# Kernel tuning notes

Hardware: AMD Instinct MI355X
Metric: run time of the kernel (lower is better)

Reference implementation:

```python
import jax, jax.numpy as jnp
import numpy as np

EPS = 1e-5

def conv1x1(x, W, b):
    # x: [B,Cin,H,W], W: [Cout,Cin], b: [Cout] -> [B,Cout,H,W]
    return jnp.einsum('oc,bchw->bohw', W, x) + b[None, :, None, None]

def setup_inputs() -> dict:
    key = jax.random.key(0)
    ks = jax.random.split(key, 12)
    C, Ci = 256, 128
    B, Hh, Wh, Hl, Wl = 8, 32, 32, 64, 64
    sc = 1.0 / np.sqrt(C)
    sci = 1.0 / np.sqrt(Ci)
    return {
        'x_high': jax.random.normal(ks[0], (B, C, Hh, Wh), jnp.float32),
        'x_low':  jax.random.normal(ks[1], (B, C, Hl, Wl), jnp.float32),
        'Wg': jax.random.normal(ks[2], (Ci, C), jnp.float32) * sc,
        'bg': jax.random.normal(ks[3], (Ci,), jnp.float32) * 0.01,
        'Wt': jax.random.normal(ks[4], (Ci, C), jnp.float32) * sc,
        'bt': jax.random.normal(ks[5], (Ci,), jnp.float32) * 0.01,
        'Wp': jax.random.normal(ks[6], (Ci, C), jnp.float32) * sc,
        'bp': jax.random.normal(ks[7], (Ci,), jnp.float32) * 0.01,
        'Wz': jax.random.normal(ks[8], (C, Ci), jnp.float32) * sci,
        'bz': jax.random.normal(ks[9], (C,), jnp.float32) * 0.01,
        'gamma': jnp.ones((C,), jnp.float32),
        'beta': jnp.zeros((C,), jnp.float32),
    }

def reference(x_high, x_low, Wg, bg, Wt, bt, Wp, bp, Wz, bz, gamma, beta):
    B, C, Hl, Wl = x_low.shape
    Ci = Wg.shape[0]
    Nh = x_high.shape[2] * x_high.shape[3]
    Nl = Hl * Wl
    # 1x1 conv projections (pure channel GEMMs)
    g_x = conv1x1(x_high, Wg, bg).reshape(B, Ci, Nh).transpose(0, 2, 1)    # [B,Nh,Ci]
    theta_x = conv1x1(x_low, Wt, bt).reshape(B, Ci, Nl).transpose(0, 2, 1) # [B,Nl,Ci]
    phi_x = conv1x1(x_high, Wp, bp).reshape(B, Ci, Nh)                     # [B,Ci,Nh]
    # unnormalized attention (no softmax), scaled by number of key positions
    f = jnp.matmul(theta_x, phi_x)            # [B,Nl,Nh]
    y = jnp.matmul(f / Nh, g_x)               # [B,Nl,Ci]
    y = y.transpose(0, 2, 1).reshape(B, Ci, Hl, Wl)
    # W_z: 1x1 conv then GroupNorm(num_groups=1) -> layernorm over (C,H,W) per sample
    z = conv1x1(y, Wz, bz)                    # [B,C,Hl,Wl]
    mu = jnp.mean(z, axis=(1, 2, 3), keepdims=True)
    var = jnp.var(z, axis=(1, 2, 3), keepdims=True)
    z = (z - mu) * jax.lax.rsqrt(var + EPS)
    z = z * gamma[None, :, None, None] + beta[None, :, None, None]
    return z
```

## Files before the change

kernel.cpp:

```cpp
#include <hip/hip_runtime.h>
#include <hip/hip_bf16.h>

typedef __attribute__((ext_vector_type(8))) short bf16x8;
typedef __attribute__((ext_vector_type(4))) float f32x4;
typedef __attribute__((ext_vector_type(8))) unsigned short us8;

#define MFMA(a, b, c) __builtin_amdgcn_mfma_f32_16x16x32_bf16(a, b, c, 0, 0, 0)

__device__ inline unsigned short f2bf(float f) {
  unsigned u = __builtin_bit_cast(unsigned, f);
  u += 0x7FFF + ((u >> 16) & 1);
  return (unsigned short)(u >> 16);
}
__device__ inline float bf2f(unsigned short s) {
  unsigned u = ((unsigned)s) << 16;
  return __builtin_bit_cast(float, u);
}
__device__ inline unsigned pack2(float lo, float hi) {
  return (unsigned)f2bf(lo) | ((unsigned)f2bf(hi) << 16);
}
__device__ inline void gll16(const unsigned short* gsrc, unsigned short* ldst) {
  __builtin_amdgcn_global_load_lds(
      (const __attribute__((address_space(1))) unsigned int*)gsrc,
      (__attribute__((address_space(3))) unsigned int*)ldst, 16, 0, 0);
}

__global__ __launch_bounds__(256) void proj_f2(
    const float* __restrict__ xh,
    const float* __restrict__ Wp, const float* __restrict__ bp,
    const float* __restrict__ Wg, const float* __restrict__ bg,
    unsigned short* __restrict__ phi,
    unsigned short* __restrict__ gg) {
  __shared__ unsigned short Bs[64 * 256];
  __shared__ unsigned short As[2][64 * 64];
  const int b = blockIdx.x, i0 = blockIdx.y * 64, n0 = blockIdx.z * 64;
  const int t = threadIdx.x, lane = t & 63;
  const int wid = t >> 6, wr = wid >> 1, wc = wid & 1;
  #pragma unroll
  for (int it = 0; it < 8; ++it) {
    int s = it * 256 + t;
    int nf = (s & 7) | ((s >> 10) << 3);
    int c2 = (s >> 3) & 127;
    const float* p = xh + ((size_t)(b * 256 + 2 * c2)) * 1024 + n0 + nf * 4;
    float4 a = *(const float4*)p;
    float4 bq = *(const float4*)(p + 1024);
    const float* ap = (const float*)&a;
    const float* bp2 = (const float*)&bq;
    #pragma unroll
    for (int i = 0; i < 4; ++i) {
      int n = nf * 4 + i;
      int col32 = (((c2 >> 2) ^ (n & 7)) << 2) | (c2 & 3);
      ((unsigned*)Bs)[n * 128 + col32] = pack2(ap[i], bp2[i]);
    }
  }
  f32x4 accP[2][2] = {};
  f32x4 accG[2][2] = {};
  const int ar = t >> 2, acb = (t & 3) * 16;
  for (int kt = 0; kt < 4; ++kt) {
    #pragma unroll
    for (int w = 0; w < 2; ++w) {
      const float* W = (w ? Wg : Wp) + (size_t)(i0 + ar) * 256 + kt * 64 + acb;
      #pragma unroll
      for (int q = 0; q < 4; ++q) {
        float4 v = *(const float4*)(W + q * 4);
        int cl0 = acb + q * 4;
        int c2a = cl0 >> 1, c2b = c2a + 1;
        int sa = (((c2a >> 2) ^ (ar & 7)) << 2) | (c2a & 3);
        int sb = (((c2b >> 2) ^ (ar & 7)) << 2) | (c2b & 3);
        ((unsigned*)As[w])[ar * 32 + sa] = pack2(v.x, v.y);
        ((unsigned*)As[w])[ar * 32 + sb] = pack2(v.z, v.w);
      }
    }
    __syncthreads();
    #pragma unroll
    for (int ks = 0; ks < 2; ++ks) {
      bf16x8 bfr[2];
      #pragma unroll
      for (int fm = 0; fm < 2; ++fm) {
        int r = wc * 32 + fm * 16 + (lane & 15);
        int gc = kt * 8 + ks * 4 + (lane >> 4);
        bfr[fm] = *(const bf16x8*)&Bs[r * 256 + (gc ^ (r & 7)) * 8];
      }
      #pragma unroll
      for (int fo = 0; fo < 2; ++fo) {
        int r = wr * 32 + fo * 16 + (lane & 15);
        int ga = ks * 4 + (lane >> 4);
        bf16x8 ap = *(const bf16x8*)&As[0][r * 64 + (ga ^ (r & 7)) * 8];
        bf16x8 ag = *(const bf16x8*)&As[1][r * 64 + (ga ^ (r & 7)) * 8];
        accP[fo][0] = MFMA(ap, bfr[0], accP[fo][0]);
        accP[fo][1] = MFMA(ap, bfr[1], accP[fo][1]);
        accG[fo][0] = MFMA(ag, bfr[0], accG[fo][0]);
        accG[fo][1] = MFMA(ag, bfr[1], accG[fo][1]);
      }
    }
    __syncthreads();
  }
  #pragma unroll
  for (int fo = 0; fo < 2; ++fo) {
    #pragma unroll
    for (int q = 0; q < 4; ++q) {
      int i = i0 + wr * 32 + fo * 16 + (lane >> 4) * 4 + q;
      float vp = bp[i], vg = bg[i];
      #pragma unroll
      for (int fm = 0; fm < 2; ++fm) {
        int n = n0 + wc * 32 + fm * 16 + (lane & 15);
        size_t off = ((size_t)((b * 128) + i)) * 1024 + n;
        phi[off] = f2bf(accP[fo][fm][q] + vp);
        gg[off]  = f2bf(accG[fo][fm][q] + vg);
      }
    }
  }
}

__global__ __launch_bounds__(256) void mpart_mfma(
    const unsigned short* __restrict__ phi, const unsigned short* __restrict__ gg,
    float* __restrict__ Mpart) {
  __shared__ unsigned short ps[128 * 128];
  __shared__ unsigned short gs[128 * 128];
  const int b = blockIdx.x, kc = blockIdx.y;
  const int t = threadIdx.x, lane = t & 63;
  const int wid = t >> 6, wr = wid >> 1, wc = wid & 1;
  #pragma unroll
  for (int j = 0; j < 8; ++j) {
    int slot = t + j * 256;
    int r = slot >> 4, gq = slot & 15;
    size_t src = ((size_t)(b * 128 + r)) * 1024 + kc * 128 + (gq ^ (r & 7)) * 8;
    gll16(phi + src, ps + slot * 8);
    gll16(gg + src, gs + slot * 8);
  }
  __syncthreads();
  f32x4 acc[4][4] = {};
  #pragma unroll
  for (int ks = 0; ks < 4; ++ks) {
    bf16x8 av[4], bv[4];
    #pragma unroll
    for (int f = 0; f < 4; ++f) {
      int ra = wr * 64 + f * 16 + (lane & 15);
      int rb = wc * 64 + f * 16 + (lane & 15);
      int gc = ks * 4 + (lane >> 4);
      av[f] = *(const bf16x8*)&ps[ra * 128 + (gc ^ (ra & 7)) * 8];
      bv[f] = *(const bf16x8*)&gs[rb * 128 + (gc ^ (rb & 7)) * 8];
    }
    #pragma unroll
    for (int i = 0; i < 4; ++i)
      #pragma unroll
      for (int j2 = 0; j2 < 4; ++j2)
        acc[i][j2] = MFMA(av[i], bv[j2], acc[i][j2]);
  }
  float* mp = Mpart + ((size_t)(b * 8 + kc)) * 128 * 128;
  #pragma unroll
  for (int i = 0; i < 4; ++i)
    #pragma unroll
    for (int q = 0; q < 4; ++q) {
      int ii = wr * 64 + i * 16 + (lane >> 4) * 4 + q;
      #pragma unroll
      for (int j2 = 0; j2 < 4; ++j2) {
        int jj = wc * 64 + j2 * 16 + (lane & 15);
        mp[ii * 128 + jj] = acc[i][j2][q];
      }
    }
}

__global__ __launch_bounds__(256) void mkw2(
    const float* __restrict__ Mpart, const float* __restrict__ Wz,
    const float* __restrict__ Wt, const float* __restrict__ bt,
    const float* __restrict__ bz,
    unsigned short* __restrict__ W2b, float* __restrict__ b2) {
  __shared__ float Ms[128 * 129];
  __shared__ float Ws2[32 * 132];
  const int b = blockIdx.x, o0 = blockIdx.y * 32;
  const int t = threadIdx.x;
  #pragma unroll
  for (int q = 0; q < 4; ++q) {
    int f = t + q * 256;
    int o = f >> 5, j4 = (f & 31) * 4;
    float4 v = *(const float4*)&Wz[(size_t)(o0 + o) * 128 + j4];
    Ws2[o * 132 + j4 + 0] = v.x; Ws2[o * 132 + j4 + 1] = v.y;
    Ws2[o * 132 + j4 + 2] = v.z; Ws2[o * 132 + j4 + 3] = v.w;
  }
  #pragma unroll
  for (int q = 0; q < 16; ++q) {
    int f = t + q * 256;
    const float4* p = (const float4*)(Mpart + (size_t)b * 8 * 16384) + f;
    float4 s = p[0];
    #pragma unroll
    for (int kc = 1; kc < 8; ++kc) {
      float4 v = p[(size_t)kc * 4096];
      s.x += v.x; s.y += v.y; s.z += v.z; s.w += v.w;
    }
    const float sc = 1.0f / 1024.0f;
    int i = f >> 5, j = (f & 31) * 4;
    Ms[i * 129 + j + 0] = s.x * sc; Ms[i * 129 + j + 1] = s.y * sc;
    Ms[i * 129 + j + 2] = s.z * sc; Ms[i * 129 + j + 3] = s.w * sc;
  }
  __syncthreads();
  const int i = t & 127, oh = t >> 7;
  float k2[16] = {};
  for (int j = 0; j < 128; ++j) {
    float m = Ms[i * 129 + j];
    #pragma unroll
    for (int oo = 0; oo < 16; ++oo)
      k2[oo] += m * Ws2[(oh * 16 + oo) * 132 + j];
  }
  __syncthreads();
  #pragma unroll
  for (int oo = 0; oo < 16; ++oo)
    Ws2[(oh * 16 + oo) * 132 + i] = k2[oo];
  __syncthreads();
  const int c = t;
  float acc[32] = {};
  for (int i2 = 0; i2 < 128; ++i2) {
    float wt = Wt[(size_t)i2 * 256 + c];
    #pragma unroll
    for (int o = 0; o < 32; ++o)
      acc[o] += wt * Ws2[o * 132 + i2];
  }
  #pragma unroll
  for (int o = 0; o < 32; ++o)
    W2b[((size_t)(b * 256 + o0 + o)) * 256 + c] = f2bf(acc[o]);
  if (t < 32) {
    float s = 0.f;
    for (int i2 = 0; i2 < 128; ++i2) s += Ws2[t * 132 + i2] * bt[i2];
    b2[b * 256 + o0 + t] = s + bz[o0 + t];
  }
}

__global__ __launch_bounds__(256) void mk_z_f(
    const float* __restrict__ xl,
    const unsigned short* __restrict__ W2b,
    const float* __restrict__ b2,
    unsigned short* __restrict__ z,
    float* __restrict__ sums) {
  __shared__ unsigned short As[256 * 64];
  __shared__ unsigned short Bs[32 * 64];
  __shared__ float red[8];
  const int b = blockIdx.x, m0 = blockIdx.y * 32;
  const int t = threadIdx.x, lane = t & 63;
  const int w = t >> 6;
  const int mf = t & 7, c2 = t >> 3;
  f32x4 acc[4][2] = {};
  for (int kt = 0; kt < 4; ++kt) {
    #pragma unroll
    for (int j = 0; j < 8; ++j) {
      int slot = t + j * 256;
      int r = slot >> 3, gq = slot & 7;
      gll16(W2b + ((size_t)(b * 256 + r)) * 256 + kt * 64 + (gq ^ (r & 7)) * 8,
            As + slot * 8);
    }
    {
      const float* p = xl + ((size_t)(b * 256 + kt * 64 + 2 * c2)) * 4096 + m0 + mf * 4;
      float4 a = *(const float4*)p;
      float4 bq = *(const float4*)(p + 4096);
      const float* ap = (const float*)&a;
      const float* bp2 = (const float*)&bq;
      #pragma unroll
      for (int i = 0; i < 4; ++i) {
        int m = mf * 4 + i;
        int col32 = (((c2 >> 2) ^ (m & 7)) << 2) | (c2 & 3);
        ((unsigned*)Bs)[m * 32 + col32] = pack2(ap[i], bp2[i]);
      }
    }
    __syncthreads();
    #pragma unroll
    for (int ks = 0; ks < 2; ++ks) {
      bf16x8 av[4], bv[2];
      #pragma unroll
      for (int f = 0; f < 2; ++f) {
        int rb = f * 16 + (lane & 15);
        int gc = ks * 4 + (lane >> 4);
        bv[f] = *(const bf16x8*)&Bs[rb * 64 + (gc ^ (rb & 7)) * 8];
      }
      #pragma unroll
      for (int f = 0; f < 4; ++f) {
        int ra = w * 64 + f * 16 + (lane & 15);
        int gc = ks * 4 + (lane >> 4);
        av[f] = *(const bf16x8*)&As[ra * 64 + (gc ^ (ra & 7)) * 8];
      }
      #pragma unroll
      for (int i = 0; i < 4; ++i)
        #pragma unroll
        for (int j2 = 0; j2 < 2; ++j2)
          acc[i][j2] = MFMA(av[i], bv[j2], acc[i][j2]);
    }
    __syncthreads();
  }
  float ls = 0.f, ls2 = 0.f;
  #pragma unroll
  for (int i = 0; i < 4; ++i) {
    #pragma unroll
    for (int q = 0; q < 4; ++q) {
      int o = w * 64 + i * 16 + (lane >> 4) * 4 + q;
      float bias = b2[b * 256 + o];
      #pragma unroll
      for (int j2 = 0; j2 < 2; ++j2) {
        int m = m0 + j2 * 16 + (lane & 15);
        float v = acc[i][j2][q] + bias;
        z[((size_t)(b * 256 + o)) * 4096 + m] = f2bf(v);
        ls += v; ls2 += v * v;
      }
    }
  }
  #pragma unroll
  for (int off = 32; off > 0; off >>= 1) {
    ls  += __shfl_down(ls, off);
    ls2 += __shfl_down(ls2, off);
  }
  if ((t & 63) == 0) { red[w * 2] = ls; red[w * 2 + 1] = ls2; }
  __syncthreads();
  if (t == 0) {
    atomicAdd(&sums[b * 2 + 0], red[0] + red[2] + red[4] + red[6]);
    atomicAdd(&sums[b * 2 + 1], red[1] + red[3] + red[5] + red[7]);
  }
}

__global__ __launch_bounds__(256) void ln_out(
    const unsigned short* __restrict__ z, const float* __restrict__ sums,
    const float* __restrict__ gamma, const float* __restrict__ beta,
    float* __restrict__ out) {
  size_t i8 = (size_t)blockIdx.x * 256 + threadIdx.x;
  int b = (int)(i8 >> 17);
  int o = (int)((i8 >> 9) & 255);
  float s = sums[b * 2], s2 = sums[b * 2 + 1];
  const float invN = 1.0f / (256.0f * 4096.0f);
  float mu = s * invN;
  float var = s2 * invN - mu * mu;
  float rs = rsqrtf(var + 1e-5f);
  float ga = gamma[o] * rs;
  float be = beta[o] - mu * rs * gamma[o];
  us8 u = *(const us8*)&z[i8 * 8];
  float4 r0, r1;
  r0.x = bf2f(u[0]) * ga + be; r0.y = bf2f(u[1]) * ga + be;
  r0.z = bf2f(u[2]) * ga + be; r0.w = bf2f(u[3]) * ga + be;
  r1.x = bf2f(u[4]) * ga + be; r1.y = bf2f(u[5]) * ga + be;
  r1.z = bf2f(u[6]) * ga + be; r1.w = bf2f(u[7]) * ga + be;
  *(float4*)&out[i8 * 8] = r0;
  *(float4*)&out[i8 * 8 + 4] = r1;
}

extern "C" void kernel_launch(void* const* d_in, const int* in_sizes, int n_in,
                              void* d_out, int out_size, void* d_ws, size_t ws_size,
                              hipStream_t stream) {
  const float* xh    = (const float*)d_in[0];
  const float* xl    = (const float*)d_in[1];
  const float* Wg    = (const float*)d_in[2];
  const float* bg    = (const float*)d_in[3];
  const float* Wt    = (const float*)d_in[4];
  const float* bt    = (const float*)d_in[5];
  const float* Wp    = (const float*)d_in[6];
  const float* bp    = (const float*)d_in[7];
  const float* Wz    = (const float*)d_in[8];
  const float* bz    = (const float*)d_in[9];
  const float* gamma = (const float*)d_in[10];
  const float* beta  = (const float*)d_in[11];
  float* out = (float*)d_out;
  float* ws = (float*)d_ws;

  unsigned short* phi  = (unsigned short*)(ws + 0);
  unsigned short* gbuf = (unsigned short*)(ws + 524288);
  float* Mpart = ws + 1048576;
  unsigned short* zbuf = (unsigned short*)(ws + 0);
  unsigned short* W2b  = (unsigned short*)(ws + 4194304);
  float* b2    = ws + 4456448;
  float* sums  = ws + 4458496;

  hipMemsetAsync(sums, 0, 16 * sizeof(float), stream);

  proj_f2<<<dim3(8, 2, 16), 256, 0, stream>>>(xh, Wp, bp, Wg, bg, phi, gbuf);
  mpart_mfma<<<dim3(8, 8), 256, 0, stream>>>(phi, gbuf, Mpart);
  mkw2<<<dim3(8, 8), 256, 0, stream>>>(Mpart, Wz, Wt, bt, bz, W2b, b2);
  mk_z_f<<<dim3(8, 128), 256, 0, stream>>>(xl, W2b, b2, zbuf, sums);
  ln_out<<<4096, 256, 0, stream>>>(zbuf, sums, gamma, beta, out);
}
```

Before: 209.2 us.

## Split Mpart reduction and compute W2 products with bf16 MFMA

The scalar fp32 mkw2 kernel is replaced by two kernels. The first reduces the eight Mpart partial sums into a swizzled bf16 M matrix. The second computes K2 = Wz·M and W2 = K2·Wt with MFMA instructions from swizzled LDS tiles, and derives b2 from K2. This targets the scalar FMA loops that were serialized inside 64 blocks, at the cost of an extra launch, extra bf16 rounding of the intermediates, and only 16 blocks in the MFMA kernel.

```diff
diff --git a/kernel.cpp b/kernel.cpp
--- a/kernel.cpp
+++ b/kernel.cpp
@@ -3,6 +3,7 @@
 
 typedef __attribute__((ext_vector_type(8))) short bf16x8;
 typedef __attribute__((ext_vector_type(4))) float f32x4;
+typedef __attribute__((ext_vector_type(4))) unsigned short us4;
 typedef __attribute__((ext_vector_type(8))) unsigned short us8;
 
 #define MFMA(a, b, c) __builtin_amdgcn_mfma_f32_16x16x32_bf16(a, b, c, 0, 0, 0)
@@ -161,67 +162,157 @@
     }
 }
 
-__global__ __launch_bounds__(256) void mkw2(
-    const float* __restrict__ Mpart, const float* __restrict__ Wz,
-    const float* __restrict__ Wt, const float* __restrict__ bt,
-    const float* __restrict__ bz,
+__global__ __launch_bounds__(256) void mreduce_bf(
+    const float* __restrict__ Mpart, unsigned short* __restrict__ M_bf) {
+  int f = blockIdx.x * 256 + threadIdx.x;
+  int b = f >> 12, r = f & 4095;
+  const float4* p = (const float4*)Mpart + (size_t)b * 32768 + r;
+  float4 s = p[0];
+  #pragma unroll
+  for (int kc = 1; kc < 8; ++kc) {
+    float4 v = p[(size_t)kc * 4096];
+    s.x += v.x; s.y += v.y; s.z += v.z; s.w += v.w;
+  }
+  const float sc = 1.0f / 1024.0f;
+  us4 o;
+  o[0] = f2bf(s.x * sc); o[1] = f2bf(s.y * sc);
+  o[2] = f2bf(s.z * sc); o[3] = f2bf(s.w * sc);
+  int i = r >> 5, j4 = r & 31;
+  int gsw = (j4 >> 1) ^ (i & 7);
+  *(us4*)&M_bf[((size_t)(b * 128 + i)) * 128 + gsw * 8 + (j4 & 1) * 4] = o;
+}
+
+__global__ __launch_bounds__(256) void k2w2_mfma(
+    const unsigned short* __restrict__ M_bf,
+    const float* __restrict__ Wz, const float* __restrict__ Wt,
+    const float* __restrict__ bt, const float* __restrict__ bz,
     unsigned short* __restrict__ W2b, float* __restrict__ b2) {
-  __shared__ float Ms[128 * 129];
-  __shared__ float Ws2[32 * 132];
-  const int b = blockIdx.x, o0 = blockIdx.y * 32;
-  const int t = threadIdx.x;
-  #pragma unroll
-  for (int q = 0; q < 4; ++q) {
-    int f = t + q * 256;
-    int o = f >> 5, j4 = (f & 31) * 4;
-    float4 v = *(const float4*)&Wz[(size_t)(o0 + o) * 128 + j4];
-    Ws2[o * 132 + j4 + 0] = v.x; Ws2[o * 132 + j4 + 1] = v.y;
-    Ws2[o * 132 + j4 + 2] = v.z; Ws2[o * 132 + j4 + 3] = v.w;
-  }
-  #pragma unroll
-  for (int q = 0; q < 16; ++q) {
-    int f = t + q * 256;
-    const float4* p = (const float4*)(Mpart + (size_t)b * 8 * 16384) + f;
-    float4 s = p[0];
-    #pragma unroll
-    for (int kc = 1; kc < 8; ++kc) {
-      float4 v = p[(size_t)kc * 4096];
-      s.x += v.x; s.y += v.y; s.z += v.z; s.w += v.w;
-    }
-    const float sc = 1.0f / 1024.0f;
-    int i = f >> 5, j = (f & 31) * 4;
-    Ms[i * 129 + j + 0] = s.x * sc; Ms[i * 129 + j + 1] = s.y * sc;
-    Ms[i * 129 + j + 2] = s.z * sc; Ms[i * 129 + j + 3] = s.w * sc;
+  __shared__ unsigned short Wz_s[128 * 128];
+  __shared__ unsigned short M_s[128 * 128];
+  __shared__ unsigned short K2_s[128 * 128];
+  __shared__ unsigned short Wt_s[128 * 128];
+  const int b = blockIdx.x, o0 = blockIdx.y * 128;
+  const int t = threadIdx.x, lane = t & 63;
+  const int w = t >> 6;
+  #pragma unroll
+  for (int it = 0; it < 16; ++it) {
+    int f = it * 256 + t;
+    int r = f >> 5, j4 = f & 31;
+    float4 v = *(const float4*)&Wz[(size_t)(o0 + r) * 128 + j4 * 4];
+    us4 o;
+    o[0] = f2bf(v.x); o[1] = f2bf(v.y); o[2] = f2bf(v.z); o[3] = f2bf(v.w);
+    int gsw = (j4 >> 1) ^ (r & 7);
+    *(us4*)&Wz_s[r * 128 + gsw * 8 + (j4 & 1) * 4] = o;
+  }
+  #pragma unroll
+  for (int j = 0; j < 8; ++j) {
+    int slot = t + j * 256;
+    int r = slot >> 4, gq = slot & 15;
+    gll16(M_bf + ((size_t)(b * 128 + r)) * 128 + gq * 8, M_s + slot * 8);
   }
   __syncthreads();
-  const int i = t & 127, oh = t >> 7;
-  float k2[16] = {};
-  for (int j = 0; j < 128; ++j) {
-    float m = Ms[i * 129 + j];
-    #pragma unroll
-    for (int oo = 0; oo < 16; ++oo)
-      k2[oo] += m * Ws2[(oh * 16 + oo) * 132 + j];
+  f32x4 acc1[2][8] = {};
+  #pragma unroll
+  for (int ks = 0; ks < 4; ++ks) {
+    int gc = ks * 4 + (lane >> 4);
+    bf16x8 av[2], bv[8];
+    #pragma unroll
+    for (int fo = 0; fo < 2; ++fo) {
+      int ro = w * 32 + fo * 16 + (lane & 15);
+      av[fo] = *(const bf16x8*)&Wz_s[ro * 128 + (gc ^ (ro & 7)) * 8];
+    }
+    #pragma unroll
+    for (int fi = 0; fi < 8; ++fi) {
+      int ri = fi * 16 + (lane & 15);
+      bv[fi] = *(const bf16x8*)&M_s[ri * 128 + (gc ^ (ri & 7)) * 8];
+    }
+    #pragma unroll
+    for (int fo = 0; fo < 2; ++fo)
+      #pragma unroll
+      for (int fi = 0; fi < 8; ++fi)
+        acc1[fo][fi] = MFMA(av[fo], bv[fi], acc1[fo][fi]);
+  }
+  #pragma unroll
+  for (int fo = 0; fo < 2; ++fo)
+    #pragma unroll
+    for (int q = 0; q < 4; ++q) {
+      int ol = w * 32 + fo * 16 + (lane >> 4) * 4 + q;
+      #pragma unroll
+      for (int fi = 0; fi < 8; ++fi) {
+        int i = fi * 16 + (lane & 15);
+        K2_s[ol * 128 + (((i >> 3) ^ (ol & 7)) * 8) + (i & 7)] =
+            f2bf(acc1[fo][fi][q]);
+      }
+    }
+  #pragma unroll
+  for (int it = 0; it < 16; ++it) {
+    int f = it * 256 + t;
+    int cl = f & 127, iq = (f >> 7) & 31;
+    int i0 = iq * 4;
+    us4 o;
+    o[0] = f2bf(Wt[(size_t)(i0 + 0) * 256 + cl]);
+    o[1] = f2bf(Wt[(size_t)(i0 + 1) * 256 + cl]);
+    o[2] = f2bf(Wt[(size_t)(i0 + 2) * 256 + cl]);
+    o[3] = f2bf(Wt[(size_t)(i0 + 3) * 256 + cl]);
+    *(us4*)&Wt_s[cl * 128 + (((i0 >> 3) ^ (cl & 7)) * 8) + (i0 & 7)] = o;
   }
   __syncthreads();
-  #pragma unroll
-  for (int oo = 0; oo < 16; ++oo)
-    Ws2[(oh * 16 + oo) * 132 + i] = k2[oo];
-  __syncthreads();
-  const int c = t;
-  float acc[32] = {};
-  for (int i2 = 0; i2 < 128; ++i2) {
-    float wt = Wt[(size_t)i2 * 256 + c];
-    #pragma unroll
-    for (int o = 0; o < 32; ++o)
-      acc[o] += wt * Ws2[o * 132 + i2];
-  }
-  #pragma unroll
-  for (int o = 0; o < 32; ++o)
-    W2b[((size_t)(b * 256 + o0 + o)) * 256 + c] = f2bf(acc[o]);
-  if (t < 32) {
+  if (t < 128) {
     float s = 0.f;
-    for (int i2 = 0; i2 < 128; ++i2) s += Ws2[t * 132 + i2] * bt[i2];
+    for (int i = 0; i < 128; ++i)
+      s += bf2f(K2_s[t * 128 + (((i >> 3) ^ (t & 7)) * 8) + (i & 7)]) * bt[i];
     b2[b * 256 + o0 + t] = s + bz[o0 + t];
+  }
+  #pragma unroll
+  for (int cc = 0; cc < 2; ++cc) {
+    f32x4 acc2[2][8] = {};
+    #pragma unroll
+    for (int ks = 0; ks < 4; ++ks) {
+      int gc = ks * 4 + (lane >> 4);
+      bf16x8 av[2], bv[8];
+      #pragma unroll
+      for (int fo = 0; fo < 2; ++fo) {
+        int ro = w * 32 + fo * 16 + (lane & 15);
+        av[fo] = *(const bf16x8*)&K2_s[ro * 128 + (gc ^ (ro & 7)) * 8];
+      }
+      #pragma unroll
+      for (int fc = 0; fc < 8; ++fc) {
+        int rc = fc * 16 + (lane & 15);
+        bv[fc] = *(const bf16x8*)&Wt_s[rc * 128 + (gc ^ (rc & 7)) * 8];
+      }
+      #pragma unroll
+      for (int fo = 0; fo < 2; ++fo)
+        #pragma unroll
+        for (int fc = 0; fc < 8; ++fc)
+          acc2[fo][fc] = MFMA(av[fo], bv[fc], acc2[fo][fc]);
+    }
+    #pragma unroll
+    for (int fo = 0; fo < 2; ++fo)
+      #pragma unroll
+      for (int q = 0; q < 4; ++q) {
+        int o = o0 + w * 32 + fo * 16 + (lane >> 4) * 4 + q;
+        #pragma unroll
+        for (int fc = 0; fc < 8; ++fc) {
+          int c = cc * 128 + fc * 16 + (lane & 15);
+          W2b[((size_t)(b * 256 + o)) * 256 + c] = f2bf(acc2[fo][fc][q]);
+        }
+      }
+    if (cc == 0) {
+      __syncthreads();
+      #pragma unroll
+      for (int it = 0; it < 16; ++it) {
+        int f = it * 256 + t;
+        int cl = f & 127, iq = (f >> 7) & 31;
+        int i0 = iq * 4;
+        us4 o;
+        o[0] = f2bf(Wt[(size_t)(i0 + 0) * 256 + 128 + cl]);
+        o[1] = f2bf(Wt[(size_t)(i0 + 1) * 256 + 128 + cl]);
+        o[2] = f2bf(Wt[(size_t)(i0 + 2) * 256 + 128 + cl]);
+        o[3] = f2bf(Wt[(size_t)(i0 + 3) * 256 + 128 + cl]);
+        *(us4*)&Wt_s[cl * 128 + (((i0 >> 3) ^ (cl & 7)) * 8) + (i0 & 7)] = o;
+      }
+      __syncthreads();
+    }
   }
 }
 
@@ -358,6 +449,7 @@
   unsigned short* phi  = (unsigned short*)(ws + 0);
   unsigned short* gbuf = (unsigned short*)(ws + 524288);
   float* Mpart = ws + 1048576;
+  unsigned short* M_bf = (unsigned short*)(ws + 2097152);
   unsigned short* zbuf = (unsigned short*)(ws + 0);
   unsigned short* W2b  = (unsigned short*)(ws + 4194304);
   float* b2    = ws + 4456448;
@@ -367,7 +459,8 @@
 
   proj_f2<<<dim3(8, 2, 16), 256, 0, stream>>>(xh, Wp, bp, Wg, bg, phi, gbuf);
   mpart_mfma<<<dim3(8, 8), 256, 0, stream>>>(phi, gbuf, Mpart);
-  mkw2<<<dim3(8, 8), 256, 0, stream>>>(Mpart, Wz, Wt, bt, bz, W2b, b2);
+  mreduce_bf<<<128, 256, 0, stream>>>(Mpart, M_bf);
+  k2w2_mfma<<<dim3(8, 2), 256, 0, stream>>>(M_bf, Wz, Wt, bt, bz, W2b, b2);
   mk_z_f<<<dim3(8, 128), 256, 0, stream>>>(xl, W2b, b2, zbuf, sums);
   ln_out<<<4096, 256, 0, stream>>>(zbuf, sums, gamma, beta, out);
 }
```

Measured after the change: 178.6 us. -14.6%, faster.
